# Performance work log

Hardware: AMD Instinct MI355X
Metric: run time of the kernel (lower is better)

The kernel has to match this reference:

```python
import jax, jax.numpy as jnp
import numpy as np

N = 8192

def gcn_conv(x, edge_index, W, b):
    # PyG GCNConv: x' = D^{-1/2} (A + I) D^{-1/2} (x W) + b
    n = x.shape[0]
    loops = jnp.arange(n, dtype=edge_index.dtype)
    src = jnp.concatenate([edge_index[0], loops])
    dst = jnp.concatenate([edge_index[1], loops])
    h = x @ W  # transform first (as PyG does): [n, out]
    deg = jax.ops.segment_sum(jnp.ones_like(dst, dtype=h.dtype), dst, num_segments=n)
    dinv = jnp.where(deg > 0, jax.lax.rsqrt(deg), 0.0)
    norm = dinv[src] * dinv[dst]  # [E+n]
    out = jax.ops.segment_sum(norm[:, None] * h[src], dst, num_segments=n)
    return out + b


def setup_inputs() -> dict:
    key = jax.random.key(0)
    ks = jax.random.split(key, 9)
    F, H = 512, 512
    E = 262144
    x = jax.random.normal(ks[0], (N, F), dtype=jnp.float32)
    o = jax.random.normal(ks[1], (N, 4), dtype=jnp.float32)
    edge_index = jax.random.randint(ks[2], (2, E), 0, N, dtype=jnp.int64)
    s = 1.0 / np.sqrt(F)
    W1 = jax.random.uniform(ks[3], (F, H), jnp.float32, -s, s)
    b1 = jnp.zeros((H,), jnp.float32)
    s2 = 1.0 / np.sqrt(H)
    W2 = jax.random.uniform(ks[4], (H, 1), jnp.float32, -s2, s2)
    b2 = jnp.zeros((1,), jnp.float32)
    Wl = jax.random.uniform(ks[5], (4, 1), jnp.float32, -0.5, 0.5)
    bl = jnp.zeros((1,), jnp.float32)
    return {"x": x, "o": o, "edge_index": edge_index,
            "W1": W1, "b1": b1, "W2": W2, "b2": b2, "Wl": Wl, "bl": bl}


def reference(x, o, edge_index, W1, b1, W2, b2, Wl, bl):
    h = gcn_conv(x, edge_index, W1, b1)
    h = jax.nn.relu(h)
    h = gcn_conv(h, edge_index, W2, b2)  # [N, 1]
    h = h.mean(axis=1)                    # [N]
    ohe = o @ Wl + bl                      # [N, 1]
    # faithful to torch: [N] + [N,1] broadcasts to [N,N]
    return h + ohe
```

## Files before the change

### kernel.cpp

```cpp
#include <hip/hip_runtime.h>

#define NN 8192
#define FI 512
#define FH 512

typedef __attribute__((ext_vector_type(8))) short short8;
typedef __attribute__((ext_vector_type(4))) float f32x4;
typedef __attribute__((ext_vector_type(2))) float f32x2;

__device__ __forceinline__ unsigned short f2bf(float f) {
    unsigned u = __float_as_uint(f);
    unsigned r = (u + 0x7fff + ((u >> 16) & 1)) >> 16;
    return (unsigned short)r;
}

#define GLOAD_LDS16(g, l)                                                        \
    __builtin_amdgcn_global_load_lds((__attribute__((address_space(1))) const void*)(g), \
                                     (__attribute__((address_space(3))) void*)(l), 16, 0, 0)

__global__ __launch_bounds__(256) void k_prep(const float* __restrict__ x,
                                              const float* __restrict__ W1,
                                              unsigned short* __restrict__ xb,
                                              unsigned short* __restrict__ W1t,
                                              int* __restrict__ deg,
                                              int* __restrict__ cursor) {
    int b = blockIdx.x, t = threadIdx.x;
    if (b < 1024) {
        #pragma unroll
        for (int u = 0; u < 4; ++u) {
            int i = (b * 4 + u) * 256 + t;
            float4 v = reinterpret_cast<const float4*>(x)[i];
            ushort4 h;
            h.x = f2bf(v.x); h.y = f2bf(v.y); h.z = f2bf(v.z); h.w = f2bf(v.w);
            reinterpret_cast<ushort4*>(xb)[i] = h;
        }
    } else if (b < 1088) {
        __shared__ float tile[64][65];
        int bi = (b - 1024) >> 3;
        int bj = (b - 1024) & 7;
        int c = t & 63, r0 = t >> 6;
        #pragma unroll
        for (int rr = 0; rr < 16; ++rr) {
            int row = rr * 4 + r0;
            tile[row][c] = W1[(size_t)(bi * 64 + row) * FH + bj * 64 + c];
        }
        __syncthreads();
        #pragma unroll
        for (int rr = 0; rr < 16; ++rr) {
            int row = rr * 4 + r0;
            W1t[(size_t)(bj * 64 + row) * FI + bi * 64 + c] = f2bf(tile[c][row]);
        }
    } else {
        int i = (b - 1088) * 256 + t;
        deg[i] = 0; cursor[i] = 0;
    }
}

__global__ void k_deg(const int* __restrict__ dst, int E, int* __restrict__ deg) {
    int i = blockIdx.x * blockDim.x + threadIdx.x;
    if (i < E) atomicAdd(&deg[dst[i]], 1);
}

__global__ __launch_bounds__(1024) void k_scan(const int* __restrict__ deg,
                                               int* __restrict__ row_ptr,
                                               float* __restrict__ dinv) {
    __shared__ int lds[1024];
    int tid = threadIdx.x;
    int base = tid * 8;
    int l[8]; int s = 0;
    #pragma unroll
    for (int u = 0; u < 8; ++u) {
        l[u] = deg[base + u] + 1;
        dinv[base + u] = rsqrtf((float)l[u]);
        s += l[u];
    }
    lds[tid] = s;
    __syncthreads();
    for (int off = 1; off < 1024; off <<= 1) {
        int add = (tid >= off) ? lds[tid - off] : 0;
        __syncthreads();
        lds[tid] += add;
        __syncthreads();
    }
    int run = lds[tid] - s;
    #pragma unroll
    for (int u = 0; u < 8; ++u) { row_ptr[base + u] = run; run += l[u]; }
    if (tid == 1023) row_ptr[NN] = lds[1023];
}

__global__ void k_fill(const int* __restrict__ src, const int* __restrict__ dst, int E,
                       const float* __restrict__ dinv, const int* __restrict__ row_ptr,
                       int* __restrict__ cursor, int2* __restrict__ csr) {
    int i = blockIdx.x * blockDim.x + threadIdx.x;
    if (i < E) {
        int s = src[i], d = dst[i];
        int p = row_ptr[d] + atomicAdd(&cursor[d], 1);
        csr[p] = make_int2(s, __float_as_int(dinv[s] * dinv[d]));
    } else if (i < E + NN) {
        int v = i - E;
        int p = row_ptr[v] + atomicAdd(&cursor[v], 1);
        csr[p] = make_int2(v, __float_as_int(dinv[v] * dinv[v]));
    }
}

__global__ __launch_bounds__(256) void k_gemm(const unsigned short* __restrict__ xb,
                                              const unsigned short* __restrict__ W1t,
                                              unsigned char* __restrict__ h8) {
    __shared__ __align__(16) unsigned short As[64 * 64];
    __shared__ __align__(16) unsigned short Bs[64 * 64];
    int tid  = threadIdx.x;
    int lane = tid & 63;
    int wave = tid >> 6;
    int wm = wave >> 1, wn = wave & 1;
    int bm = blockIdx.y * 64, bn = blockIdx.x * 64;

    f32x4 acc[2][2] = {};

    int r  = lane & 15;
    int s0 = lane >> 4;

    for (int kt = 0; kt < FI / 64; ++kt) {
        #pragma unroll
        for (int t = 0; t < 2; ++t) {
            int q   = t * 256 + tid;
            int row = q >> 3;
            int sl  = q & 7;
            int sg  = sl ^ (row & 7);
            GLOAD_LDS16(xb  + (size_t)(bm + row) * FI + kt * 64 + sg * 8, As + q * 8);
            GLOAD_LDS16(W1t + (size_t)(bn + row) * FI + kt * 64 + sg * 8, Bs + q * 8);
        }
        __syncthreads();

        #pragma unroll
        for (int kc = 0; kc < 2; ++kc) {
            short8 a[2], b[2];
            #pragma unroll
            for (int m = 0; m < 2; ++m) {
                int row = wm * 32 + m * 16 + r;
                int sl  = (kc * 4 + s0) ^ (row & 7);
                a[m] = *reinterpret_cast<const short8*>(As + row * 64 + sl * 8);
            }
            #pragma unroll
            for (int n = 0; n < 2; ++n) {
                int row = wn * 32 + n * 16 + r;
                int sl  = (kc * 4 + s0) ^ (row & 7);
                b[n] = *reinterpret_cast<const short8*>(Bs + row * 64 + sl * 8);
            }
            #pragma unroll
            for (int m = 0; m < 2; ++m)
                #pragma unroll
                for (int n = 0; n < 2; ++n)
                    acc[m][n] = __builtin_amdgcn_mfma_f32_16x16x32_bf16(a[m], b[n], acc[m][n], 0, 0, 0);
        }
        __syncthreads();
    }

    #pragma unroll
    for (int m = 0; m < 2; ++m) {
        #pragma unroll
        for (int n = 0; n < 2; ++n) {
            int col = bn + wn * 32 + n * 16 + (lane & 15);
            int rw0 = bm + wm * 32 + m * 16 + (lane >> 4) * 4;
            #pragma unroll
            for (int reg = 0; reg < 4; ++reg) {
                float v = acc[m][n][reg];
                int pk = __builtin_amdgcn_cvt_pk_fp8_f32(v, v, 0, false);
                h8[(size_t)(rw0 + reg) * FH + col] = (unsigned char)(pk & 0xff);
            }
        }
    }
}

__device__ __forceinline__ void accp(f32x2* __restrict__ acc, uint2 rv, float w) {
    f32x2 wv = {w, w};
    acc[0] += wv * __builtin_amdgcn_cvt_pk_f32_fp8((int)rv.x, false);
    acc[1] += wv * __builtin_amdgcn_cvt_pk_f32_fp8((int)rv.x, true);
    acc[2] += wv * __builtin_amdgcn_cvt_pk_f32_fp8((int)rv.y, false);
    acc[3] += wv * __builtin_amdgcn_cvt_pk_f32_fp8((int)rv.y, true);
}

__global__ __launch_bounds__(256) void k_agg(const unsigned char* __restrict__ h8,
                                             const int* __restrict__ row_ptr,
                                             const int2* __restrict__ csr,
                                             const float* __restrict__ b1,
                                             const float* __restrict__ W2,
                                             float* __restrict__ z) {
    int lane = threadIdx.x & 63;
    int v = blockIdx.x * 4 + (threadIdx.x >> 6);
    f32x2 acc[4] = {};
    int p0 = row_ptr[v], p1 = row_ptr[v + 1];
    for (int base = p0; base < p1; base += 64) {
        int cnt = p1 - base; if (cnt > 64) cnt = 64;
        int2 sw = (lane < cnt) ? csr[base + lane] : make_int2(0, 0);
        int j = 0;
        for (; j + 4 <= cnt; j += 4) {
            int   s0 = __shfl(sw.x, j),     s1 = __shfl(sw.x, j + 1);
            int   s2 = __shfl(sw.x, j + 2), s3 = __shfl(sw.x, j + 3);
            float w0 = __int_as_float(__shfl(sw.y, j));
            float w1 = __int_as_float(__shfl(sw.y, j + 1));
            float w2 = __int_as_float(__shfl(sw.y, j + 2));
            float w3 = __int_as_float(__shfl(sw.y, j + 3));
            uint2 r0 = *reinterpret_cast<const uint2*>(h8 + (size_t)s0 * FH + lane * 8);
            uint2 r1 = *reinterpret_cast<const uint2*>(h8 + (size_t)s1 * FH + lane * 8);
            uint2 r2 = *reinterpret_cast<const uint2*>(h8 + (size_t)s2 * FH + lane * 8);
            uint2 r3 = *reinterpret_cast<const uint2*>(h8 + (size_t)s3 * FH + lane * 8);
            accp(acc, r0, w0);
            accp(acc, r1, w1);
            accp(acc, r2, w2);
            accp(acc, r3, w3);
        }
        for (; j < cnt; ++j) {
            int   sj = __shfl(sw.x, j);
            float wj = __int_as_float(__shfl(sw.y, j));
            uint2 rj = *reinterpret_cast<const uint2*>(h8 + (size_t)sj * FH + lane * 8);
            accp(acc, rj, wj);
        }
    }
    const f32x2* b2p = reinterpret_cast<const f32x2*>(b1 + lane * 8);
    const f32x2* w2p = reinterpret_cast<const f32x2*>(W2 + lane * 8);
    float val = 0.f;
    #pragma unroll
    for (int q = 0; q < 4; ++q) {
        f32x2 t = acc[q] + b2p[q];
        t.x = fmaxf(t.x, 0.f);
        t.y = fmaxf(t.y, 0.f);
        f32x2 r = t * w2p[q];
        val += r.x + r.y;
    }
    #pragma unroll
    for (int off = 32; off; off >>= 1) val += __shfl_down(val, off);
    if (lane == 0) z[v] = val;
}

__global__ void k_node(const float* __restrict__ z,
                       const int* __restrict__ row_ptr,
                       const int2* __restrict__ csr,
                       const float* __restrict__ b2,
                       const float* __restrict__ o,
                       const float* __restrict__ Wl,
                       const float* __restrict__ bl,
                       float* __restrict__ h2, float* __restrict__ ohe) {
    int v = blockIdx.x * blockDim.x + threadIdx.x;
    if (v >= NN) return;
    float acc = 0.f;
    int p1 = row_ptr[v + 1];
    for (int p = row_ptr[v]; p < p1; ++p) {
        int2 sw = csr[p];
        acc += __int_as_float(sw.y) * z[sw.x];
    }
    h2[v] = acc + b2[0];
    float4 ov = *reinterpret_cast<const float4*>(&o[(size_t)v * 4]);
    ohe[v] = ov.x * Wl[0] + ov.y * Wl[1] + ov.z * Wl[2] + ov.w * Wl[3] + bl[0];
}

__global__ __launch_bounds__(256) void k_out(const float* __restrict__ h2,
                                             const float* __restrict__ ohe,
                                             float4* __restrict__ out) {
    int i0 = blockIdx.x * 4;
    int t  = threadIdx.x;
    float4 h[8];
    #pragma unroll
    for (int u = 0; u < 8; ++u) h[u] = reinterpret_cast<const float4*>(h2)[u * 256 + t];
    #pragma unroll
    for (int rr = 0; rr < 4; ++rr) {
        float oi = ohe[i0 + rr];
        float4* dst = out + (size_t)(i0 + rr) * 2048;
        #pragma unroll
        for (int u = 0; u < 8; ++u) {
            float4 v = h[u];
            dst[u * 256 + t] = make_float4(v.x + oi, v.y + oi, v.z + oi, v.w + oi);
        }
    }
}

extern "C" void kernel_launch(void* const* d_in, const int* in_sizes, int n_in,
                              void* d_out, int out_size, void* d_ws, size_t ws_size,
                              hipStream_t stream) {
    const float* x  = (const float*)d_in[0];
    const float* o  = (const float*)d_in[1];
    const int*   ei = (const int*)d_in[2];
    const float* W1 = (const float*)d_in[3];
    const float* b1 = (const float*)d_in[4];
    const float* W2 = (const float*)d_in[5];
    const float* b2 = (const float*)d_in[6];
    const float* Wl = (const float*)d_in[7];
    const float* bl = (const float*)d_in[8];
    float* out = (float*)d_out;

    const int E = in_sizes[2] / 2;
    const int* src = ei;
    const int* dst = ei + E;

    char* p = (char*)d_ws;
    auto alloc = [&](size_t bytes) {
        char* r = p;
        p += (bytes + 255) & ~(size_t)255;
        return r;
    };
    int*   deg     = (int*)  alloc(NN * 4);
    float* dinv    = (float*)alloc(NN * 4);
    int*   row_ptr = (int*)  alloc((NN + 1) * 4);
    int*   cursor  = (int*)  alloc(NN * 4);
    int2*  csr     = (int2*) alloc((size_t)(E + NN) * 8);
    unsigned short* xb  = (unsigned short*)alloc((size_t)NN * FI * 2);
    unsigned short* W1t = (unsigned short*)alloc((size_t)FH * FI * 2);
    unsigned char*  h8  = (unsigned char*) alloc((size_t)NN * FH);
    float* z       = (float*)alloc(NN * 4);
    float* h2      = (float*)alloc(NN * 4);
    float* ohe     = (float*)alloc(NN * 4);

    k_prep <<<1120, 256, 0, stream>>>(x, W1, xb, W1t, deg, cursor);
    k_deg  <<<(E + 255) / 256, 256, 0, stream>>>(dst, E, deg);
    k_scan <<<1, 1024, 0, stream>>>(deg, row_ptr, dinv);
    k_fill <<<(E + NN + 255) / 256, 256, 0, stream>>>(src, dst, E, dinv, row_ptr, cursor, csr);
    k_gemm <<<dim3(FH / 64, NN / 64), 256, 0, stream>>>(xb, W1t, h8);
    k_agg  <<<NN / 4, 256, 0, stream>>>(h8, row_ptr, csr, b1, W2, z);
    k_node <<<(NN + 255) / 256, 256, 0, stream>>>(z, row_ptr, csr, b2, o, Wl, bl, h2, ohe);
    k_out  <<<NN / 4, 256, 0, stream>>>(h2, ohe, (float4*)out);
}
```

Baseline: 141.1 us.

## Merge degree counting into prep kernel and CSR fill into GEMM launch

The degree atomics move into the x/W1 conversion kernel, and the CSR fill becomes extra blocks of the GEMM kernel, so independent work shares a single launch. Zeroing of deg and cursor moves to a small separate kernel, which relies on the two arrays being allocated contiguously. This removes launch gaps and lets the atomic-heavy fill overlap with the matrix multiply. The cost is a more complex kernel layout and a dependency on the buffer ordering.

```diff
diff --git a/kernel.cpp b/kernel.cpp
--- a/kernel.cpp
+++ b/kernel.cpp
@@ -18,12 +18,16 @@
     __builtin_amdgcn_global_load_lds((__attribute__((address_space(1))) const void*)(g), \
                                      (__attribute__((address_space(3))) void*)(l), 16, 0, 0)
 
-__global__ __launch_bounds__(256) void k_prep(const float* __restrict__ x,
-                                              const float* __restrict__ W1,
-                                              unsigned short* __restrict__ xb,
-                                              unsigned short* __restrict__ W1t,
-                                              int* __restrict__ deg,
-                                              int* __restrict__ cursor) {
+__global__ void k_zero(int* __restrict__ zero_base) {
+    zero_base[blockIdx.x * 256 + threadIdx.x] = 0;
+}
+
+__global__ __launch_bounds__(256) void k_prepdeg(const float* __restrict__ x,
+                                                 const float* __restrict__ W1,
+                                                 const int* __restrict__ dstE, int E,
+                                                 unsigned short* __restrict__ xb,
+                                                 unsigned short* __restrict__ W1t,
+                                                 int* __restrict__ deg) {
     int b = blockIdx.x, t = threadIdx.x;
     if (b < 1024) {
         #pragma unroll
@@ -52,13 +56,8 @@
         }
     } else {
         int i = (b - 1088) * 256 + t;
-        deg[i] = 0; cursor[i] = 0;
-    }
-}
-
-__global__ void k_deg(const int* __restrict__ dst, int E, int* __restrict__ deg) {
-    int i = blockIdx.x * blockDim.x + threadIdx.x;
-    if (i < E) atomicAdd(&deg[dst[i]], 1);
+        if (i < E) atomicAdd(&deg[dstE[i]], 1);
+    }
 }
 
 __global__ __launch_bounds__(1024) void k_scan(const int* __restrict__ deg,
@@ -88,34 +87,40 @@
     if (tid == 1023) row_ptr[NN] = lds[1023];
 }
 
-__global__ void k_fill(const int* __restrict__ src, const int* __restrict__ dst, int E,
-                       const float* __restrict__ dinv, const int* __restrict__ row_ptr,
-                       int* __restrict__ cursor, int2* __restrict__ csr) {
-    int i = blockIdx.x * blockDim.x + threadIdx.x;
-    if (i < E) {
-        int s = src[i], d = dst[i];
-        int p = row_ptr[d] + atomicAdd(&cursor[d], 1);
-        csr[p] = make_int2(s, __float_as_int(dinv[s] * dinv[d]));
-    } else if (i < E + NN) {
-        int v = i - E;
-        int p = row_ptr[v] + atomicAdd(&cursor[v], 1);
-        csr[p] = make_int2(v, __float_as_int(dinv[v] * dinv[v]));
-    }
-}
-
-__global__ __launch_bounds__(256) void k_gemm(const unsigned short* __restrict__ xb,
-                                              const unsigned short* __restrict__ W1t,
-                                              unsigned char* __restrict__ h8) {
+__global__ __launch_bounds__(256) void k_fillgemm(const int* __restrict__ srcE,
+                                                  const int* __restrict__ dstE, int E,
+                                                  const float* __restrict__ dinv,
+                                                  const int* __restrict__ row_ptr,
+                                                  int* __restrict__ cursor,
+                                                  int2* __restrict__ csr,
+                                                  const unsigned short* __restrict__ xb,
+                                                  const unsigned short* __restrict__ W1t,
+                                                  unsigned char* __restrict__ h8) {
     __shared__ __align__(16) unsigned short As[64 * 64];
     __shared__ __align__(16) unsigned short Bs[64 * 64];
-    int tid  = threadIdx.x;
+    int bid = blockIdx.x, tid = threadIdx.x;
+
+    if (bid < 1056) {
+        int i = bid * 256 + tid;
+        if (i < E) {
+            int s = srcE[i], d = dstE[i];
+            int p = row_ptr[d] + atomicAdd(&cursor[d], 1);
+            csr[p] = make_int2(s, __float_as_int(dinv[s] * dinv[d]));
+        } else if (i < E + NN) {
+            int v = i - E;
+            int p = row_ptr[v] + atomicAdd(&cursor[v], 1);
+            csr[p] = make_int2(v, __float_as_int(dinv[v] * dinv[v]));
+        }
+        return;
+    }
+
+    int q0 = bid - 1056;
     int lane = tid & 63;
     int wave = tid >> 6;
     int wm = wave >> 1, wn = wave & 1;
-    int bm = blockIdx.y * 64, bn = blockIdx.x * 64;
+    int bm = (q0 >> 3) * 64, bn = (q0 & 7) * 64;
 
     f32x4 acc[2][2] = {};
-
     int r  = lane & 15;
     int s0 = lane >> 4;
 
@@ -298,9 +303,9 @@
         return r;
     };
     int*   deg     = (int*)  alloc(NN * 4);
+    int*   cursor  = (int*)  alloc(NN * 4);
     float* dinv    = (float*)alloc(NN * 4);
     int*   row_ptr = (int*)  alloc((NN + 1) * 4);
-    int*   cursor  = (int*)  alloc(NN * 4);
     int2*  csr     = (int2*) alloc((size_t)(E + NN) * 8);
     unsigned short* xb  = (unsigned short*)alloc((size_t)NN * FI * 2);
     unsigned short* W1t = (unsigned short*)alloc((size_t)FH * FI * 2);
@@ -309,12 +314,12 @@
     float* h2      = (float*)alloc(NN * 4);
     float* ohe     = (float*)alloc(NN * 4);
 
-    k_prep <<<1120, 256, 0, stream>>>(x, W1, xb, W1t, deg, cursor);
-    k_deg  <<<(E + 255) / 256, 256, 0, stream>>>(dst, E, deg);
-    k_scan <<<1, 1024, 0, stream>>>(deg, row_ptr, dinv);
-    k_fill <<<(E + NN + 255) / 256, 256, 0, stream>>>(src, dst, E, dinv, row_ptr, cursor, csr);
-    k_gemm <<<dim3(FH / 64, NN / 64), 256, 0, stream>>>(xb, W1t, h8);
-    k_agg  <<<NN / 4, 256, 0, stream>>>(h8, row_ptr, csr, b1, W2, z);
-    k_node <<<(NN + 255) / 256, 256, 0, stream>>>(z, row_ptr, csr, b2, o, Wl, bl, h2, ohe);
-    k_out  <<<NN / 4, 256, 0, stream>>>(h2, ohe, (float4*)out);
-}
+    k_zero    <<<64, 256, 0, stream>>>(deg);
+    k_prepdeg <<<1088 + (E + 255) / 256, 256, 0, stream>>>(x, W1, dst, E, xb, W1t, deg);
+    k_scan    <<<1, 1024, 0, stream>>>(deg, row_ptr, dinv);
+    k_fillgemm<<<1056 + 1024, 256, 0, stream>>>(src, dst, E, dinv, row_ptr, cursor, csr,
+                                                xb, W1t, h8);
+    k_agg     <<<NN / 4, 256, 0, stream>>>(h8, row_ptr, csr, b1, W2, z);
+    k_node    <<<(NN + 255) / 256, 256, 0, stream>>>(z, row_ptr, csr, b2, o, Wl, bl, h2, ohe);
+    k_out     <<<NN / 4, 256, 0, stream>>>(h2, ohe, (float4*)out);
+}
```

After: 132.9 us. -5.8%, faster.
